# Kernel optimization log

Hardware: AMD Instinct MI355X
Metric: run time of the kernel (lower is better)

Reference implementation:

```python
import jax, jax.numpy as jnp
import numpy as np

V = 32000      # vocab_size
CTX = 1024     # context_length
D = 768        # n_embd
H = 12         # n_heads
HD = D // H    # head_dim
L = 6          # n_layers
DFF = 4 * D
B, S = 2, 1024
EPS = 1e-5


def _layernorm(x, w, b):
    mu = jnp.mean(x, axis=-1, keepdims=True)
    var = jnp.mean(jnp.square(x - mu), axis=-1, keepdims=True)
    return (x - mu) * jax.lax.rsqrt(var + EPS) * w + b


def setup_inputs() -> dict:
    key = jax.random.key(0)
    ks = iter(jax.random.split(key, 32))
    s = 0.02
    idx = jax.random.randint(next(ks), (B, S), 0, V)
    p = {
        "idx": idx,
        "tok_emb": jax.random.normal(next(ks), (V, D), jnp.float32) * s,
        "pos_emb": jax.random.normal(next(ks), (CTX, D), jnp.float32) * s,
        "ln1_w": jnp.ones((L, D)), "ln1_b": jnp.zeros((L, D)),
        "Wq": jax.random.normal(next(ks), (L, D, D), jnp.float32) * s,
        "bq": jnp.zeros((L, D)),
        "Wk": jax.random.normal(next(ks), (L, D, D), jnp.float32) * s,
        "bk": jnp.zeros((L, D)),
        "Wv": jax.random.normal(next(ks), (L, D, D), jnp.float32) * s,
        "bv": jnp.zeros((L, D)),
        "Wo": jax.random.normal(next(ks), (L, D, D), jnp.float32) * s,
        "bo": jnp.zeros((L, D)),
        "ln2_w": jnp.ones((L, D)), "ln2_b": jnp.zeros((L, D)),
        "W1": jax.random.normal(next(ks), (L, D, DFF), jnp.float32) * s,
        "b1": jnp.zeros((L, DFF)),
        "W2": jax.random.normal(next(ks), (L, DFF, D), jnp.float32) * s,
        "b2": jnp.zeros((L, D)),
        "lnf_w": jnp.ones((D,)), "lnf_b": jnp.zeros((D,)),
        "lm_head_w": jax.random.normal(next(ks), (D, V), jnp.float32) * s,
    }
    return p


def _forward(idx, tok_emb, pos_emb, ln1_w, ln1_b, Wq, bq, Wk, bk, Wv, bv,
             Wo, bo, ln2_w, ln2_b, W1, b1, W2, b2, lnf_w, lnf_b, lm_head_w):
    b, s = idx.shape
    x = tok_emb[idx] + pos_emb[:s]  # [B,S,D]
    mask = jnp.tril(jnp.ones((s, s), dtype=bool))  # causal
    scale = 1.0 / np.sqrt(HD)
    for l in range(L):
        # --- attention ---
        h = _layernorm(x, ln1_w[l], ln1_b[l])
        q = (h @ Wq[l] + bq[l]).reshape(b, s, H, HD).transpose(0, 2, 1, 3)
        k = (h @ Wk[l] + bk[l]).reshape(b, s, H, HD).transpose(0, 2, 1, 3)
        v = (h @ Wv[l] + bv[l]).reshape(b, s, H, HD).transpose(0, 2, 1, 3)
        att = jnp.einsum('bhqd,bhkd->bhqk', q, k) * scale
        att = jnp.where(mask, att, -jnp.inf)
        att = jax.nn.softmax(att, axis=-1)
        y = jnp.einsum('bhqk,bhkd->bhqd', att, v)
        y = y.transpose(0, 2, 1, 3).reshape(b, s, D)
        x = x + y @ Wo[l] + bo[l]
        # --- MLP ---
        h2 = _layernorm(x, ln2_w[l], ln2_b[l])
        x = x + jax.nn.relu(h2 @ W1[l] + b1[l]) @ W2[l] + b2[l]
    logits = _layernorm(x, lnf_w, lnf_b) @ lm_head_w  # [B,S,V]
    return logits


def reference(idx, tok_emb, pos_emb, ln1_w, ln1_b, Wq, bq, Wk, bk, Wv, bv,
              Wo, bo, ln2_w, ln2_b, W1, b1, W2, b2, lnf_w, lnf_b, lm_head_w):
    return _forward(idx, tok_emb, pos_emb, ln1_w, ln1_b, Wq, bq, Wk, bk, Wv,
                    bv, Wo, bo, ln2_w, ln2_b, W1, b1, W2, b2, lnf_w, lnf_b,
                    lm_head_w)
```

## Files before the change

### kernel.cpp

```cpp
#include <hip/hip_runtime.h>
#include <hip/hip_bf16.h>
#include <math.h>

#define D 768
#define NH 12
#define HD 64
#define NL 6
#define DFF 3072
#define BB 2
#define SS 1024
#define NROWS (BB*SS)
#define VOCAB 32000
#define QKVN (3*D)
#define LN_EPS 1e-5f

typedef __attribute__((ext_vector_type(8))) short bf16x8;
typedef __attribute__((ext_vector_type(4))) float f32x4;

typedef __attribute__((address_space(1))) const unsigned char* gas_ptr;
typedef __attribute__((address_space(3))) unsigned char* las_ptr;

__device__ __forceinline__ void load_lds16(const void* g, void* l) {
    __builtin_amdgcn_global_load_lds((gas_ptr)g, (las_ptr)l, 16, 0, 0);
}

__device__ __forceinline__ void storeOut(float* p, float v) { *p = v; }
__device__ __forceinline__ void storeOut(__hip_bfloat16* p, float v) { *p = __float2bfloat16(v); }
__device__ __forceinline__ ushort f2bs(float f) {
    __hip_bfloat16 h = __float2bfloat16(f);
    return *(ushort*)&h;
}

__global__ void embed_kernel(const int* __restrict__ idx, const float* __restrict__ tok,
                             const float* __restrict__ pos, float* __restrict__ x) {
    int row = blockIdx.x;
    int s = row % SS;
    int t = idx[row];
    for (int c = threadIdx.x; c < D; c += blockDim.x)
        x[row*D + c] = tok[(size_t)t*D + c] + pos[s*D + c];
}

template<typename OT>
__global__ __launch_bounds__(256) void layernorm_kernel(const float* __restrict__ x,
                                                        const float* __restrict__ w,
                                                        const float* __restrict__ b,
                                                        OT* __restrict__ out) {
    int row = blockIdx.x;
    __shared__ float l1[4], l2[4];
    int base = row * D;
    float vals[3];
    float s1 = 0.f, s2 = 0.f;
#pragma unroll
    for (int i = 0; i < 3; i++) {
        float v = x[base + threadIdx.x + i*256];
        vals[i] = v; s1 += v; s2 += v*v;
    }
#pragma unroll
    for (int o = 32; o > 0; o >>= 1) {
        s1 += __shfl_down(s1, o, 64);
        s2 += __shfl_down(s2, o, 64);
    }
    if ((threadIdx.x & 63) == 0) { l1[threadIdx.x >> 6] = s1; l2[threadIdx.x >> 6] = s2; }
    __syncthreads();
    float sum   = l1[0] + l1[1] + l1[2] + l1[3];
    float sumsq = l2[0] + l2[1] + l2[2] + l2[3];
    float mu  = sum * (1.f / D);
    float var = sumsq * (1.f / D) - mu * mu;
    float inv = rsqrtf(var + LN_EPS);
#pragma unroll
    for (int i = 0; i < 3; i++) {
        int c = threadIdx.x + i*256;
        storeOut(&out[base + c], (vals[i] - mu) * inv * w[c] + b[c]);
    }
}

__global__ __launch_bounds__(256) void transpose_cvt(const float* __restrict__ src,
                                                     __hip_bfloat16* __restrict__ dst,
                                                     int K, int N,
                                                     size_t srcLayerStride, size_t dstLayerStride,
                                                     int dstRowOff) {
    int l = blockIdx.z;
    src += (size_t)l * srcLayerStride;
    dst += (size_t)l * dstLayerStride + (size_t)dstRowOff * K;
    __shared__ float t[32][33];
    int k0 = blockIdx.x*32, n0 = blockIdx.y*32;
    int tx = threadIdx.x & 31, ty = threadIdx.x >> 5;
    for (int i = ty; i < 32; i += 8) t[i][tx] = src[(size_t)(k0+i)*N + n0+tx];
    __syncthreads();
    for (int i = ty; i < 32; i += 8) dst[(size_t)(n0+i)*K + k0+tx] = __float2bfloat16(t[tx][i]);
}

__global__ __launch_bounds__(256) void vtrans_kernel(const ushort* __restrict__ qkv,
                                                     ushort* __restrict__ vt) {
    int bh = blockIdx.z;
    int st = blockIdx.y;
    int dt = blockIdx.x;
    __shared__ ushort t[32][33];
    int tx = threadIdx.x & 31, ty = threadIdx.x >> 5;
    int b = bh / NH, h = bh % NH;
    int s0 = st*32, d0 = dt*32;
    for (int i = ty; i < 32; i += 8)
        t[i][tx] = qkv[(size_t)(b*SS + s0+i)*QKVN + 2*D + h*HD + d0 + tx];
    __syncthreads();
    for (int i = ty; i < 32; i += 8)
        vt[((size_t)bh*HD + d0+i)*SS + s0 + tx] = t[tx][i];
}

__global__ void pack_qkv_bias(const float* __restrict__ bq, const float* __restrict__ bk,
                              const float* __restrict__ bv, float* __restrict__ dst) {
    int l = blockIdx.y;
    int i = blockIdx.x*256 + threadIdx.x;
    dst[l*QKVN + i]         = bq[l*D + i];
    dst[l*QKVN + D + i]     = bk[l*D + i];
    dst[l*QKVN + 2*D + i]   = bv[l*D + i];
}

template<int BM, int BN, int CMAJ, typename OT, int RELU, int RESID, int HASB>
__global__ __launch_bounds__(256) void gemm_mfma(const ushort* __restrict__ A,
                                                 const ushort* __restrict__ BT,
                                                 const float* __restrict__ bias,
                                                 const float* __restrict__ X,
                                                 OT* __restrict__ C,
                                                 int N, int K, int gx, int gy) {
    constexpr int WTM = BM/2, WTN = BN/2;
    constexpr int FRM = BM/32, FRN = BN/32;
    __shared__ ushort As[BM][32];
    __shared__ ushort Bs[BN][32];

    int id = blockIdx.x;
    int swz = (id & 7) * (gridDim.x >> 3) + (id >> 3);
    int bx, by;
    if (CMAJ) { bx = swz / gy; by = swz - bx * gy; }
    else      { by = swz / gx; bx = swz - by * gx; }
    int bm = by * BM, bn = bx * BN;

    int tid = threadIdx.x;
    int lane = tid & 63, wid = tid >> 6;
    int wr = wid >> 1, wc = wid & 1;
    int lrow = lane >> 2;
    int lcol = (((lane & 3) ^ (lrow & 3)) * 8);
    int fr = lane & 15, fc = lane >> 4;

    f32x4 acc[FRM][FRN];
#pragma unroll
    for (int i = 0; i < FRM; i++)
#pragma unroll
        for (int j = 0; j < FRN; j++)
#pragma unroll
            for (int r = 0; r < 4; r++) acc[i][j][r] = 0.f;

    for (int k0 = 0; k0 < K; k0 += 32) {
#pragma unroll
        for (int i = 0; i < BM/64; i++) {
            int rt = wid*(BM/4) + i*16;
            load_lds16(A + (size_t)(bm + rt + lrow)*K + k0 + lcol, &As[rt][0]);
        }
#pragma unroll
        for (int i = 0; i < BN/64; i++) {
            int rt = wid*(BN/4) + i*16;
            load_lds16(BT + (size_t)(bn + rt + lrow)*K + k0 + lcol, &Bs[rt][0]);
        }
        asm volatile("s_waitcnt vmcnt(0)" ::: "memory");
        __syncthreads();
        bf16x8 af[FRM], bf[FRN];
#pragma unroll
        for (int mi = 0; mi < FRM; mi++)
            af[mi] = *(const bf16x8*)&As[wr*WTM + mi*16 + fr][(fc ^ (fr & 3))*8];
#pragma unroll
        for (int ni = 0; ni < FRN; ni++)
            bf[ni] = *(const bf16x8*)&Bs[wc*WTN + ni*16 + fr][(fc ^ (fr & 3))*8];
#pragma unroll
        for (int mi = 0; mi < FRM; mi++)
#pragma unroll
            for (int ni = 0; ni < FRN; ni++)
                acc[mi][ni] = __builtin_amdgcn_mfma_f32_16x16x32_bf16(af[mi], bf[ni], acc[mi][ni], 0, 0, 0);
        __syncthreads();
    }
#pragma unroll
    for (int mi = 0; mi < FRM; mi++) {
#pragma unroll
        for (int r = 0; r < 4; r++) {
            int row = bm + wr*WTM + mi*16 + fc*4 + r;
#pragma unroll
            for (int ni = 0; ni < FRN; ni++) {
                int col = bn + wc*WTN + ni*16 + fr;
                float v = acc[mi][ni][r];
                if (HASB) v += bias[col];
                if (RESID) v += X[(size_t)row * N + col];
                if (RELU) v = fmaxf(v, 0.f);
                storeOut(&C[(size_t)row * N + col], v);
            }
        }
    }
}

__global__ __launch_bounds__(256) void attn_mfma(const ushort* __restrict__ qkv,
                                                 const ushort* __restrict__ vt,
                                                 __hip_bfloat16* __restrict__ y) {
    const int bx = blockIdx.x;
    const int qt = 15 - (bx & 15);
    const int h  = (bx >> 4) % NH;
    const int b  = bx / (16*NH);
    const int tid  = threadIdx.x;
    const int lane = tid & 63, w = tid >> 6;
    const int fr = lane & 15, fc = lane >> 4;

    __shared__ ushort Qs[64][64];
    __shared__ ushort Ks[64][64];
    __shared__ ushort Vs[64][64];
    __shared__ ushort Ps[4][16][72];

    const int q0 = qt * 64;
    const int srow8  = lane >> 3;
    const int schunk = (lane & 7) ^ srow8;

#pragma unroll
    for (int j = 0; j < 2; j++) {
        int r = w*16 + j*8 + srow8;
        load_lds16(qkv + (size_t)(b*SS + q0 + r)*QKVN + h*HD + schunk*8, &Qs[w*16 + j*8][0]);
    }
    asm volatile("s_waitcnt vmcnt(0)" ::: "memory");
    bf16x8 qf[2];
#pragma unroll
    for (int s = 0; s < 2; s++)
        qf[s] = *(const bf16x8*)&Qs[w*16 + fr][((s*4 + fc) ^ (fr & 7))*8];

    f32x4 oacc[4];
#pragma unroll
    for (int ni = 0; ni < 4; ni++)
#pragma unroll
        for (int r = 0; r < 4; r++) oacc[ni][r] = 0.f;
    float m[4] = {-INFINITY, -INFINITY, -INFINITY, -INFINITY};
    float l[4] = {0.f, 0.f, 0.f, 0.f};

    for (int kt = 0; kt <= qt; kt++) {
        const int kv0 = kt * 64;
        __syncthreads();
#pragma unroll
        for (int j = 0; j < 2; j++) {
            int r = w*16 + j*8 + srow8;
            load_lds16(qkv + (size_t)(b*SS + kv0 + r)*QKVN + D + h*HD + schunk*8, &Ks[w*16 + j*8][0]);
            load_lds16(vt + ((size_t)(b*NH + h)*HD + r)*SS + kv0 + schunk*8, &Vs[w*16 + j*8][0]);
        }
        asm volatile("s_waitcnt vmcnt(0)" ::: "memory");
        __syncthreads();
        f32x4 sacc[4];
#pragma unroll
        for (int ni = 0; ni < 4; ni++)
#pragma unroll
            for (int r = 0; r < 4; r++) sacc[ni][r] = 0.f;
#pragma unroll
        for (int ni = 0; ni < 4; ni++)
#pragma unroll
            for (int s = 0; s < 2; s++) {
                bf16x8 kf = *(const bf16x8*)&Ks[ni*16 + fr][((s*4 + fc) ^ (fr & 7))*8];
                sacc[ni] = __builtin_amdgcn_mfma_f32_16x16x32_bf16(qf[s], kf, sacc[ni], 0, 0, 0);
            }
        if (kt == qt) {
#pragma unroll
            for (int ni = 0; ni < 4; ni++)
#pragma unroll
                for (int r = 0; r < 4; r++) {
                    float v = sacc[ni][r] * 0.125f;
                    sacc[ni][r] = (ni*16 + fr > w*16 + fc*4 + r) ? -INFINITY : v;
                }
        } else {
#pragma unroll
            for (int ni = 0; ni < 4; ni++)
#pragma unroll
                for (int r = 0; r < 4; r++) sacc[ni][r] *= 0.125f;
        }
        float p[4][4];
#pragma unroll
        for (int r = 0; r < 4; r++) {
            float mx = fmaxf(fmaxf(sacc[0][r], sacc[1][r]), fmaxf(sacc[2][r], sacc[3][r]));
#pragma unroll
            for (int o = 1; o < 16; o <<= 1) mx = fmaxf(mx, __shfl_xor(mx, o, 64));
            float mn = fmaxf(m[r], mx);
            float fac = __expf(m[r] - mn);
            float rs = 0.f;
#pragma unroll
            for (int ni = 0; ni < 4; ni++) {
                float pv = __expf(sacc[ni][r] - mn);
                p[ni][r] = pv;
                rs += pv;
            }
#pragma unroll
            for (int o = 1; o < 16; o <<= 1) rs += __shfl_xor(rs, o, 64);
            l[r] = l[r] * fac + rs;
            m[r] = mn;
#pragma unroll
            for (int ni = 0; ni < 4; ni++) oacc[ni][r] *= fac;
        }
#pragma unroll
        for (int ni = 0; ni < 4; ni++)
#pragma unroll
            for (int r = 0; r < 4; r++)
                Ps[w][fc*4 + r][ni*16 + fr] = f2bs(p[ni][r]);
        bf16x8 pa[2];
#pragma unroll
        for (int s = 0; s < 2; s++) pa[s] = *(const bf16x8*)&Ps[w][fr][s*32 + fc*8];
#pragma unroll
        for (int ni = 0; ni < 4; ni++)
#pragma unroll
            for (int s = 0; s < 2; s++) {
                bf16x8 vf = *(const bf16x8*)&Vs[ni*16 + fr][((s*4 + fc) ^ (fr & 7))*8];
                oacc[ni] = __builtin_amdgcn_mfma_f32_16x16x32_bf16(pa[s], vf, oacc[ni], 0, 0, 0);
            }
    }
#pragma unroll
    for (int r = 0; r < 4; r++) {
        float rinv = 1.f / l[r];
        int row = b*SS + q0 + w*16 + fc*4 + r;
#pragma unroll
        for (int ni = 0; ni < 4; ni++)
            y[(size_t)row*D + h*HD + ni*16 + fr] = __float2bfloat16(oacc[ni][r] * rinv);
    }
}

extern "C" void kernel_launch(void* const* d_in, const int* in_sizes, int n_in,
                              void* d_out, int out_size, void* d_ws, size_t ws_size,
                              hipStream_t stream) {
    const int*   idx  = (const int*)d_in[0];
    const float* tok  = (const float*)d_in[1];
    const float* pos  = (const float*)d_in[2];
    const float* ln1w = (const float*)d_in[3];
    const float* ln1b = (const float*)d_in[4];
    const float* Wq   = (const float*)d_in[5];
    const float* bq   = (const float*)d_in[6];
    const float* Wk   = (const float*)d_in[7];
    const float* bk   = (const float*)d_in[8];
    const float* Wv   = (const float*)d_in[9];
    const float* bv   = (const float*)d_in[10];
    const float* Wo   = (const float*)d_in[11];
    const float* bo   = (const float*)d_in[12];
    const float* ln2w = (const float*)d_in[13];
    const float* ln2b = (const float*)d_in[14];
    const float* W1   = (const float*)d_in[15];
    const float* b1   = (const float*)d_in[16];
    const float* W2   = (const float*)d_in[17];
    const float* b2   = (const float*)d_in[18];
    const float* lnfw = (const float*)d_in[19];
    const float* lnfb = (const float*)d_in[20];
    const float* lmw  = (const float*)d_in[21];
    float* out = (float*)d_out;

    char* p = (char*)d_ws;
    __hip_bfloat16* qkvT = (__hip_bfloat16*)p; p += (size_t)NL*QKVN*D*2;
    __hip_bfloat16* WoT  = (__hip_bfloat16*)p; p += (size_t)NL*D*D*2;
    __hip_bfloat16* W1T  = (__hip_bfloat16*)p; p += (size_t)NL*DFF*D*2;
    __hip_bfloat16* W2T  = (__hip_bfloat16*)p; p += (size_t)NL*D*DFF*2;
    __hip_bfloat16* lmT  = (__hip_bfloat16*)p; p += (size_t)VOCAB*D*2;
    float*          bqkv = (float*)p;          p += (size_t)NL*QKVN*4;
    float*          x    = (float*)p;          p += (size_t)NROWS*D*4;
    __hip_bfloat16* h    = (__hip_bfloat16*)p; p += (size_t)NROWS*D*2;
    __hip_bfloat16* qkv  = (__hip_bfloat16*)p; p += (size_t)NROWS*QKVN*2;
    __hip_bfloat16* vt   = (__hip_bfloat16*)p; p += (size_t)BB*NH*HD*SS*2;
    __hip_bfloat16* yb   = (__hip_bfloat16*)p; p += (size_t)NROWS*D*2;
    __hip_bfloat16* a1   = (__hip_bfloat16*)p; p += (size_t)NROWS*DFF*2;

    dim3 tDD(D/32, D/32, NL);
    transpose_cvt<<<tDD, 256, 0, stream>>>(Wq, qkvT, D, D, (size_t)D*D, (size_t)QKVN*D, 0);
    transpose_cvt<<<tDD, 256, 0, stream>>>(Wk, qkvT, D, D, (size_t)D*D, (size_t)QKVN*D, D);
    transpose_cvt<<<tDD, 256, 0, stream>>>(Wv, qkvT, D, D, (size_t)D*D, (size_t)QKVN*D, 2*D);
    transpose_cvt<<<tDD, 256, 0, stream>>>(Wo, WoT, D, D, (size_t)D*D, (size_t)D*D, 0);
    transpose_cvt<<<dim3(D/32, DFF/32, NL), 256, 0, stream>>>(W1, W1T, D, DFF, (size_t)D*DFF, (size_t)DFF*D, 0);
    transpose_cvt<<<dim3(DFF/32, D/32, NL), 256, 0, stream>>>(W2, W2T, DFF, D, (size_t)DFF*D, (size_t)D*DFF, 0);
    transpose_cvt<<<dim3(D/32, VOCAB/32, 1), 256, 0, stream>>>(lmw, lmT, D, VOCAB, 0, 0, 0);
    pack_qkv_bias<<<dim3(3, NL), 256, 0, stream>>>(bq, bk, bv, bqkv);

    embed_kernel<<<NROWS, 256, 0, stream>>>(idx, tok, pos, x);

    for (int l = 0; l < NL; l++) {
        layernorm_kernel<<<NROWS, 256, 0, stream>>>(x, ln1w + l*D, ln1b + l*D, h);
        gemm_mfma<128,64,0,__hip_bfloat16,0,0,1><<<576, 256, 0, stream>>>(
            (const ushort*)h, (const ushort*)(qkvT + (size_t)l*QKVN*D),
            bqkv + (size_t)l*QKVN, nullptr, qkv, QKVN, D, QKVN/64, NROWS/128);
        vtrans_kernel<<<dim3(2, SS/32, BB*NH), 256, 0, stream>>>((const ushort*)qkv, (ushort*)vt);
        attn_mfma<<<BB*NH*(SS/64), 256, 0, stream>>>((const ushort*)qkv, (const ushort*)vt, yb);
        gemm_mfma<64,64,0,float,0,1,1><<<384, 256, 0, stream>>>(
            (const ushort*)yb, (const ushort*)(WoT + (size_t)l*D*D),
            bo + (size_t)l*D, x, x, D, D, D/64, NROWS/64);
        layernorm_kernel<<<NROWS, 256, 0, stream>>>(x, ln2w + l*D, ln2b + l*D, h);
        gemm_mfma<128,128,0,__hip_bfloat16,1,0,1><<<384, 256, 0, stream>>>(
            (const ushort*)h, (const ushort*)(W1T + (size_t)l*DFF*D),
            b1 + (size_t)l*DFF, nullptr, a1, DFF, D, DFF/128, NROWS/128);
        gemm_mfma<64,64,0,float,0,1,1><<<384, 256, 0, stream>>>(
            (const ushort*)a1, (const ushort*)(W2T + (size_t)l*D*DFF),
            b2 + (size_t)l*D, x, x, D, DFF, D/64, NROWS/64);
    }
    layernorm_kernel<<<NROWS, 256, 0, stream>>>(x, lnfw, lnfb, h);
    gemm_mfma<128,128,1,float,0,0,0><<<4000, 256, 0, stream>>>(
        (const ushort*)h, (const ushort*)lmT, nullptr, nullptr, out, VOCAB, D,
        VOCAB/128, NROWS/128);
}
```

Baseline: 1.277 ms.

## Double-buffer LDS tiles in GEMM and attention kernels to overlap loads with MFMA

Both the MFMA GEMM and the flash-attention kernel now keep two LDS buffers and prefetch the next K-slice or KV tile while the current one is being computed. This leaves a single barrier per iteration instead of two and is meant to hide global-to-LDS latency behind the matrix work. The GEMM also raises wave priority with s_setprio around the MFMA block. The cost is double the LDS footprint, which may reduce occupancy, especially for the larger GEMM tiles.

```diff
diff --git a/kernel.cpp b/kernel.cpp
--- a/kernel.cpp
+++ b/kernel.cpp
@@ -115,6 +115,20 @@
     dst[l*QKVN + 2*D + i]   = bv[l*D + i];
 }
 
+#define GSTAGE(buf, k0) do {                                                     \
+    _Pragma("unroll")                                                            \
+    for (int i_ = 0; i_ < BM/64; i_++) {                                         \
+        int rt_ = wid*(BM/4) + i_*16;                                            \
+        load_lds16(A + (size_t)(bm + rt_ + lrow)*K + (k0) + lcol,                \
+                   &As[buf][rt_][0]);                                            \
+    }                                                                            \
+    _Pragma("unroll")                                                            \
+    for (int i_ = 0; i_ < BN/64; i_++) {                                         \
+        int rt_ = wid*(BN/4) + i_*16;                                            \
+        load_lds16(BT + (size_t)(bn + rt_ + lrow)*K + (k0) + lcol,               \
+                   &Bs[buf][rt_][0]);                                            \
+    } } while (0)
+
 template<int BM, int BN, int CMAJ, typename OT, int RELU, int RESID, int HASB>
 __global__ __launch_bounds__(256) void gemm_mfma(const ushort* __restrict__ A,
                                                  const ushort* __restrict__ BT,
@@ -124,8 +138,8 @@
                                                  int N, int K, int gx, int gy) {
     constexpr int WTM = BM/2, WTN = BN/2;
     constexpr int FRM = BM/32, FRN = BN/32;
-    __shared__ ushort As[BM][32];
-    __shared__ ushort Bs[BN][32];
+    __shared__ ushort As[2][BM][32];
+    __shared__ ushort Bs[2][BN][32];
 
     int id = blockIdx.x;
     int swz = (id & 7) * (gridDim.x >> 3) + (id >> 3);
@@ -149,32 +163,30 @@
 #pragma unroll
             for (int r = 0; r < 4; r++) acc[i][j][r] = 0.f;
 
-    for (int k0 = 0; k0 < K; k0 += 32) {
-#pragma unroll
-        for (int i = 0; i < BM/64; i++) {
-            int rt = wid*(BM/4) + i*16;
-            load_lds16(A + (size_t)(bm + rt + lrow)*K + k0 + lcol, &As[rt][0]);
-        }
-#pragma unroll
-        for (int i = 0; i < BN/64; i++) {
-            int rt = wid*(BN/4) + i*16;
-            load_lds16(BT + (size_t)(bn + rt + lrow)*K + k0 + lcol, &Bs[rt][0]);
-        }
+    GSTAGE(0, 0);
+    asm volatile("s_waitcnt vmcnt(0)" ::: "memory");
+    __syncthreads();
+
+    int cur = 0;
+    for (int t = 0; t < K/32; t++) {
+        if (t*32 + 32 < K) GSTAGE(cur^1, t*32 + 32);
+        bf16x8 af[FRM], bf[FRN];
+#pragma unroll
+        for (int mi = 0; mi < FRM; mi++)
+            af[mi] = *(const bf16x8*)&As[cur][wr*WTM + mi*16 + fr][(fc ^ (fr & 3))*8];
+#pragma unroll
+        for (int ni = 0; ni < FRN; ni++)
+            bf[ni] = *(const bf16x8*)&Bs[cur][wc*WTN + ni*16 + fr][(fc ^ (fr & 3))*8];
+        __builtin_amdgcn_s_setprio(1);
+#pragma unroll
+        for (int mi = 0; mi < FRM; mi++)
+#pragma unroll
+            for (int ni = 0; ni < FRN; ni++)
+                acc[mi][ni] = __builtin_amdgcn_mfma_f32_16x16x32_bf16(af[mi], bf[ni], acc[mi][ni], 0, 0, 0);
+        __builtin_amdgcn_s_setprio(0);
         asm volatile("s_waitcnt vmcnt(0)" ::: "memory");
         __syncthreads();
-        bf16x8 af[FRM], bf[FRN];
-#pragma unroll
-        for (int mi = 0; mi < FRM; mi++)
-            af[mi] = *(const bf16x8*)&As[wr*WTM + mi*16 + fr][(fc ^ (fr & 3))*8];
-#pragma unroll
-        for (int ni = 0; ni < FRN; ni++)
-            bf[ni] = *(const bf16x8*)&Bs[wc*WTN + ni*16 + fr][(fc ^ (fr & 3))*8];
-#pragma unroll
-        for (int mi = 0; mi < FRM; mi++)
-#pragma unroll
-            for (int ni = 0; ni < FRN; ni++)
-                acc[mi][ni] = __builtin_amdgcn_mfma_f32_16x16x32_bf16(af[mi], bf[ni], acc[mi][ni], 0, 0, 0);
-        __syncthreads();
+        cur ^= 1;
     }
 #pragma unroll
     for (int mi = 0; mi < FRM; mi++) {
@@ -193,6 +205,16 @@
         }
     }
 }
+
+#define KVSTAGE(buf, kv0) do {                                                   \
+    _Pragma("unroll")                                                            \
+    for (int j_ = 0; j_ < 2; j_++) {                                             \
+        int r_ = w*16 + j_*8 + srow8;                                            \
+        load_lds16(qkv + (size_t)(b*SS + (kv0) + r_)*QKVN + D + h*HD + schunk*8, \
+                   &Ks[buf][w*16 + j_*8][0]);                                    \
+        load_lds16(vt + ((size_t)(b*NH + h)*HD + r_)*SS + (kv0) + schunk*8,      \
+                   &Vs[buf][w*16 + j_*8][0]);                                    \
+    } } while (0)
 
 __global__ __launch_bounds__(256) void attn_mfma(const ushort* __restrict__ qkv,
                                                  const ushort* __restrict__ vt,
@@ -206,8 +228,8 @@
     const int fr = lane & 15, fc = lane >> 4;
 
     __shared__ ushort Qs[64][64];
-    __shared__ ushort Ks[64][64];
-    __shared__ ushort Vs[64][64];
+    __shared__ ushort Ks[2][64][64];
+    __shared__ ushort Vs[2][64][64];
     __shared__ ushort Ps[4][16][72];
 
     const int q0 = qt * 64;
@@ -219,7 +241,9 @@
         int r = w*16 + j*8 + srow8;
         load_lds16(qkv + (size_t)(b*SS + q0 + r)*QKVN + h*HD + schunk*8, &Qs[w*16 + j*8][0]);
     }
+    KVSTAGE(0, 0);
     asm volatile("s_waitcnt vmcnt(0)" ::: "memory");
+    __syncthreads();
     bf16x8 qf[2];
 #pragma unroll
     for (int s = 0; s < 2; s++)
@@ -233,17 +257,9 @@
     float m[4] = {-INFINITY, -INFINITY, -INFINITY, -INFINITY};
     float l[4] = {0.f, 0.f, 0.f, 0.f};
 
+    int cur = 0;
     for (int kt = 0; kt <= qt; kt++) {
-        const int kv0 = kt * 64;
-        __syncthreads();
-#pragma unroll
-        for (int j = 0; j < 2; j++) {
-            int r = w*16 + j*8 + srow8;
-            load_lds16(qkv + (size_t)(b*SS + kv0 + r)*QKVN + D + h*HD + schunk*8, &Ks[w*16 + j*8][0]);
-            load_lds16(vt + ((size_t)(b*NH + h)*HD + r)*SS + kv0 + schunk*8, &Vs[w*16 + j*8][0]);
-        }
-        asm volatile("s_waitcnt vmcnt(0)" ::: "memory");
-        __syncthreads();
+        if (kt < qt) KVSTAGE(cur^1, (kt+1)*64);
         f32x4 sacc[4];
 #pragma unroll
         for (int ni = 0; ni < 4; ni++)
@@ -253,7 +269,7 @@
         for (int ni = 0; ni < 4; ni++)
 #pragma unroll
             for (int s = 0; s < 2; s++) {
-                bf16x8 kf = *(const bf16x8*)&Ks[ni*16 + fr][((s*4 + fc) ^ (fr & 7))*8];
+                bf16x8 kf = *(const bf16x8*)&Ks[cur][ni*16 + fr][((s*4 + fc) ^ (fr & 7))*8];
                 sacc[ni] = __builtin_amdgcn_mfma_f32_16x16x32_bf16(qf[s], kf, sacc[ni], 0, 0, 0);
             }
         if (kt == qt) {
@@ -304,9 +320,12 @@
         for (int ni = 0; ni < 4; ni++)
 #pragma unroll
             for (int s = 0; s < 2; s++) {
-                bf16x8 vf = *(const bf16x8*)&Vs[ni*16 + fr][((s*4 + fc) ^ (fr & 7))*8];
+                bf16x8 vf = *(const bf16x8*)&Vs[cur][ni*16 + fr][((s*4 + fc) ^ (fr & 7))*8];
                 oacc[ni] = __builtin_amdgcn_mfma_f32_16x16x32_bf16(pa[s], vf, oacc[ni], 0, 0, 0);
             }
+        asm volatile("s_waitcnt vmcnt(0)" ::: "memory");
+        __syncthreads();
+        cur ^= 1;
     }
 #pragma unroll
     for (int r = 0; r < 4; r++) {
```

Result: faster. 1.246 ms (-2.4%).
